# Performance work log

Hardware: AMD Instinct MI355X
Metric: run time of the kernel (lower is better)

The kernel has to match this reference:

```python
import jax, jax.numpy as jnp
import numpy as np

B, C, H, W = 4, 512, 64, 64
C8 = C // 8


def setup_inputs() -> dict:
    key = jax.random.key(0)
    ks = jax.random.split(key, 8)
    s = 0.02
    return {
        "x": jax.random.normal(ks[0], (B, C, H, W), dtype=jnp.float32),
        "wq": jax.random.normal(ks[1], (C8, C), dtype=jnp.float32) * s,
        "bq": jax.random.normal(ks[2], (C8,), dtype=jnp.float32) * s,
        "wk": jax.random.normal(ks[3], (C8, C), dtype=jnp.float32) * s,
        "bk": jax.random.normal(ks[4], (C8,), dtype=jnp.float32) * s,
        "wv": jax.random.normal(ks[5], (C, C), dtype=jnp.float32) * s,
        "bv": jax.random.normal(ks[6], (C,), dtype=jnp.float32) * s,
        "gamma": jax.random.normal(ks[7], (1,), dtype=jnp.float32),
    }


def reference(x, wq, bq, wk, bk, wv, bv, gamma):
    b, c, h, w = x.shape
    # 1x1 convs == per-pixel linear projections
    q = jnp.einsum('bchw,oc->bohw', x, wq) + bq[None, :, None, None]  # [B,C8,H,W]
    k = jnp.einsum('bchw,oc->bohw', x, wk) + bk[None, :, None, None]  # [B,C8,H,W]
    v = jnp.einsum('bchw,oc->bohw', x, wv) + bv[None, :, None, None]  # [B,C,H,W]
    qf = q.reshape(b, c // 8, h * w)  # [B,C8,HW]
    kf = k.reshape(b, c // 8, h * w)  # [B,C8,HW]
    # energy[b,i,j] = q_i . k_j, viewed as [B,H,W,H,W]; softmax over last dim
    energy = jnp.einsum('bci,bcj->bij', qf, kf).reshape(b, h, w, h, w)
    attn = jax.nn.softmax(energy, axis=-1)  # [B,H,W,H2,W2]
    # torch: out = bmm(value, permute(0,1,3,2,4).view(B,HW,HW))
    # rows index (h,h2) into value's spatial grid; cols index output (w,w2)
    out = jnp.einsum('bchk,bhwkv->bcwv', v, attn)  # [B,C,H,W]
    return gamma * out + x
```

## Files before the change

kernel.cpp:

```cpp
#include <hip/hip_runtime.h>
#include <hip/hip_bf16.h>


typedef __bf16 bf16_t;
typedef __bf16 bf16x8 __attribute__((ext_vector_type(8)));
typedef __bf16 bf16x4 __attribute__((ext_vector_type(4)));
typedef float f32x4 __attribute__((ext_vector_type(4)));

#define HW_ 4096
#define CIN 512
#define CQ 64
#define MTOT 640

__device__ __forceinline__ void gload16(const void* g, void* l) {
  __builtin_amdgcn_global_load_lds((const __attribute__((address_space(1))) void*)g,
                                   (__attribute__((address_space(3))) void*)l, 16, 0, 0);
}

__global__ __launch_bounds__(256) void k_wcat(const float* __restrict__ wq,
                                              const float* __restrict__ wk,
                                              const float* __restrict__ wv,
                                              bf16_t* __restrict__ Wcat) {
  int idx = (blockIdx.x * 256 + threadIdx.x) * 4;
  int row = idx >> 9, c = idx & 511;
  const float* src;
  if (row < 64)       src = wq + row * 512 + c;
  else if (row < 128) src = wk + (row - 64) * 512 + c;
  else                src = wv + (row - 128) * 512 + c;
  float4 v = *(const float4*)src;
  bf16x4 o = { (bf16_t)v.x, (bf16_t)v.y, (bf16_t)v.z, (bf16_t)v.w };
  *(bf16x4*)&Wcat[idx] = o;
}

__global__ __launch_bounds__(256) void k_prep(const float* __restrict__ x, bf16_t* __restrict__ xT) {
  __shared__ float tile[64][65];
  const int b = blockIdx.z;
  const int p0 = blockIdx.x * 64, c0 = blockIdx.y * 64;
  const float* xb = x + (size_t)b * CIN * HW_;
  bf16_t* xTb = xT + (size_t)b * HW_ * CIN;
  const int tid = threadIdx.x;
  const int r = tid >> 4, q = tid & 15;
#pragma unroll
  for (int i = 0; i < 4; ++i) {
    int lr = r + 16 * i;
    float4 v = *(const float4*)&xb[(size_t)(c0 + lr) * HW_ + p0 + q * 4];
    tile[lr][q * 4 + 0] = v.x; tile[lr][q * 4 + 1] = v.y;
    tile[lr][q * 4 + 2] = v.z; tile[lr][q * 4 + 3] = v.w;
  }
  __syncthreads();
#pragma unroll
  for (int i = 0; i < 4; ++i) {
    int pr = r + 16 * i;
    bf16x4 o;
    o[0] = (bf16_t)tile[q * 4 + 0][pr];
    o[1] = (bf16_t)tile[q * 4 + 1][pr];
    o[2] = (bf16_t)tile[q * 4 + 2][pr];
    o[3] = (bf16_t)tile[q * 4 + 3][pr];
    *(bf16x4*)&xTb[(size_t)(p0 + pr) * CIN + c0 + q * 4] = o;
  }
}

__global__ __launch_bounds__(256) void k_proj(const bf16_t* __restrict__ Wcat,
                                              const bf16_t* __restrict__ xT,
                                              const float* __restrict__ bq,
                                              const float* __restrict__ bk,
                                              const float* __restrict__ bv,
                                              bf16_t* __restrict__ qfT,
                                              bf16_t* __restrict__ kfT,
                                              bf16_t* __restrict__ Vp) {
  __shared__ bf16_t As[128][64];
  __shared__ bf16_t Bs[128][64];
  const int b = blockIdx.z;
  const int m0 = blockIdx.x * 128, n0 = blockIdx.y * 128;
  const char* Wb = (const char*)Wcat;
  const char* Xb = (const char*)(xT + (size_t)b * HW_ * CIN);
  const int tid = threadIdx.x, wv_ = tid >> 6, lane = tid & 63;
  const int wm = wv_ >> 1, wn = wv_ & 1;
  f32x4 acc[4][4]{};
  for (int ks = 0; ks < 512; ks += 64) {
    if (ks) __syncthreads();
#pragma unroll
    for (int i = 0; i < 4; ++i) {
      int ch = wv_ * 4 + i;
      int rr = ch * 8 + (lane >> 3);
      gload16(Wb + (size_t)(m0 + rr) * 1024 + ks * 2 + (lane & 7) * 16, (char*)As + ch * 1024);
      gload16(Xb + (size_t)(n0 + rr) * 1024 + ks * 2 + (lane & 7) * 16, (char*)Bs + ch * 1024);
    }
    __syncthreads();
#pragma unroll
    for (int k2 = 0; k2 < 2; ++k2) {
      bf16x8 a[4], bb[4];
#pragma unroll
      for (int f = 0; f < 4; ++f)
        a[f] = *(const bf16x8*)&As[wm * 64 + f * 16 + (lane & 15)][k2 * 32 + (lane >> 4) * 8];
#pragma unroll
      for (int f = 0; f < 4; ++f)
        bb[f] = *(const bf16x8*)&Bs[wn * 64 + f * 16 + (lane & 15)][k2 * 32 + (lane >> 4) * 8];
#pragma unroll
      for (int fm = 0; fm < 4; ++fm)
#pragma unroll
        for (int fn = 0; fn < 4; ++fn)
          acc[fm][fn] = __builtin_amdgcn_mfma_f32_16x16x32_bf16(a[fm], bb[fn], acc[fm][fn], 0, 0, 0);
    }
  }
  bf16_t* qb = qfT + (size_t)b * HW_ * CQ;
  bf16_t* kb = kfT + (size_t)b * HW_ * CQ;
  bf16_t* Vb = Vp + (size_t)b * CIN * HW_;
#pragma unroll
  for (int fm = 0; fm < 4; ++fm) {
#pragma unroll
    for (int j = 0; j < 4; ++j) {
      int m = m0 + wm * 64 + fm * 16 + (lane >> 4) * 4 + j;
      float bias = (m < 64) ? bq[m] : (m < 128) ? bk[m - 64] : bv[m - 128];
#pragma unroll
      for (int fn = 0; fn < 4; ++fn) {
        int n = n0 + wn * 64 + fn * 16 + (lane & 15);
        float val = acc[fm][fn][j] + bias;
        if (m < 64)       qb[(size_t)n * CQ + m] = (bf16_t)val;
        else if (m < 128) kb[(size_t)n * CQ + (m - 64)] = (bf16_t)val;
        else              Vb[(size_t)(m - 128) * HW_ + n] = (bf16_t)val;
      }
    }
  }
}

__global__ __launch_bounds__(256) void k_energy(const bf16_t* __restrict__ qfT,
                                                const bf16_t* __restrict__ kfT,
                                                bf16_t* __restrict__ P4, int zbase) {
  __shared__ bf16_t As[128][64];
  __shared__ bf16_t Bs[64][64];
  const int b = zbase + blockIdx.z;
  const int m0 = blockIdx.x * 128, n0 = blockIdx.y * 64;
  const char* qb = (const char*)(qfT + (size_t)b * HW_ * CQ);
  const char* kb = (const char*)(kfT + (size_t)b * HW_ * CQ);
  bf16_t* Pb = P4 + (size_t)blockIdx.z * (size_t)HW_ * HW_;
  const int tid = threadIdx.x, wv_ = tid >> 6, lane = tid & 63;
  f32x4 acc[2][4]{};
#pragma unroll
  for (int i = 0; i < 4; ++i) {
    int ch = wv_ * 4 + i;
    gload16(qb + (size_t)m0 * 128 + ch * 1024 + lane * 16, (char*)As + ch * 1024);
  }
#pragma unroll
  for (int i = 0; i < 2; ++i) {
    int ch = wv_ * 2 + i;
    gload16(kb + (size_t)n0 * 128 + ch * 1024 + lane * 16, (char*)Bs + ch * 1024);
  }
  __syncthreads();
#pragma unroll
  for (int k2 = 0; k2 < 2; ++k2) {
    bf16x8 a[2], bb[4];
#pragma unroll
    for (int f = 0; f < 2; ++f)
      a[f] = *(const bf16x8*)&As[wv_ * 32 + f * 16 + (lane & 15)][k2 * 32 + (lane >> 4) * 8];
#pragma unroll
    for (int f = 0; f < 4; ++f)
      bb[f] = *(const bf16x8*)&Bs[f * 16 + (lane & 15)][k2 * 32 + (lane >> 4) * 8];
#pragma unroll
    for (int fm = 0; fm < 2; ++fm)
#pragma unroll
      for (int fn = 0; fn < 4; ++fn)
        acc[fm][fn] = __builtin_amdgcn_mfma_f32_16x16x32_bf16(a[fm], bb[fn], acc[fm][fn], 0, 0, 0);
  }
#pragma unroll
  for (int fm = 0; fm < 2; ++fm) {
#pragma unroll
    for (int j = 0; j < 4; ++j) {
      float mx = fmaxf(fmaxf(acc[fm][0][j], acc[fm][1][j]), fmaxf(acc[fm][2][j], acc[fm][3][j]));
#pragma unroll
      for (int d = 1; d < 16; d <<= 1) mx = fmaxf(mx, __shfl_xor(mx, d, 64));
      float p0 = __expf(acc[fm][0][j] - mx);
      float p1 = __expf(acc[fm][1][j] - mx);
      float p2 = __expf(acc[fm][2][j] - mx);
      float p3 = __expf(acc[fm][3][j] - mx);
      float s = p0 + p1 + p2 + p3;
#pragma unroll
      for (int d = 1; d < 16; d <<= 1) s += __shfl_xor(s, d, 64);
      float inv = __builtin_amdgcn_rcpf(s);
      size_t hw = (size_t)(m0 + wv_ * 32 + fm * 16 + (lane >> 4) * 4 + j);
      size_t base = hw * HW_ + n0 + (lane & 15);
      Pb[base + 0]  = (bf16_t)(p0 * inv);
      Pb[base + 16] = (bf16_t)(p1 * inv);
      Pb[base + 32] = (bf16_t)(p2 * inv);
      Pb[base + 48] = (bf16_t)(p3 * inv);
    }
  }
}

__global__ __launch_bounds__(256) void k_out(const bf16_t* __restrict__ Vp,
                                             const bf16_t* __restrict__ P4,
                                             const float* __restrict__ x,
                                             const float* __restrict__ gamma,
                                             float* __restrict__ outp, int zbase) {
  __shared__ char As[16384];
  __shared__ char Bs[16384];
  const int b = zbase + blockIdx.z;
  const int c0 = blockIdx.x * 128, w0 = blockIdx.y * 2;
  const char* Vb = (const char*)(Vp + (size_t)b * CIN * HW_);
  const char* Pb = (const char*)(P4 + (size_t)blockIdx.z * (size_t)HW_ * HW_);
  const int tid = threadIdx.x, wv_ = tid >> 6, lane = tid & 63;
  const int wm = wv_ >> 1, wn = wv_ & 1;
  const int g = lane >> 4, cc = lane & 15;

  const char* aS[4]; const char* bS[4]; char* aD[4]; char* bD[4];
#pragma unroll
  for (int r = 0; r < 4; ++r) {
    int L = (r * 4 + wv_) * 64 + lane;
    int arow = L >> 3, aslot = (L & 7) ^ (arow & 7);
    aS[r] = Vb + (size_t)(c0 + arow) * 8192 + aslot * 16;
    int ws = L >> 9, e = L & 511;
    int kk = e >> 3, sl = (e & 7) ^ ((kk >> 3) & 3) << 1;
    bS[r] = Pb + (size_t)(w0 + ws) * 8192 + kk * 128 + sl * 16;
    aD[r] = As + (r * 4 + wv_) * 1024;
    bD[r] = Bs + (r * 4 + wv_) * 1024;
  }
  int aoff[2][4], boff[2][4];
#pragma unroll
  for (int k2 = 0; k2 < 2; ++k2) {
#pragma unroll
    for (int fm = 0; fm < 4; ++fm)
      aoff[k2][fm] = (wm * 64 + fm * 16 + cc) * 128 + (((k2 * 4 + g) ^ (cc & 7)) * 16);
#pragma unroll
    for (int fn = 0; fn < 4; ++fn)
      boff[k2][fn] = wn * 8192 + (k2 * 32 + g * 8) * 128 + (((fn * 16 + cc) ^ (g << 4)) * 2);
  }

  f32x4 acc[4][4]{};
  for (int h = 0; h < 64; ++h) {
#pragma unroll
    for (int r = 0; r < 4; ++r) gload16(aS[r], aD[r]);
#pragma unroll
    for (int r = 0; r < 4; ++r) gload16(bS[r], bD[r]);
#pragma unroll
    for (int r = 0; r < 4; ++r) { aS[r] += 128; bS[r] += 524288; }
    __syncthreads();
#pragma unroll
    for (int k2 = 0; k2 < 2; ++k2) {
      bf16x8 a[4], bb[4];
#pragma unroll
      for (int fm = 0; fm < 4; ++fm)
        a[fm] = *(const bf16x8*)(As + aoff[k2][fm]);
#pragma unroll
      for (int fn = 0; fn < 4; ++fn) {
#pragma unroll
        for (int j = 0; j < 8; ++j)
          bb[fn][j] = *(const bf16_t*)(Bs + boff[k2][fn] + j * 128);
      }
#pragma unroll
      for (int fm = 0; fm < 4; ++fm)
#pragma unroll
        for (int fn = 0; fn < 4; ++fn)
          acc[fm][fn] = __builtin_amdgcn_mfma_f32_16x16x32_bf16(a[fm], bb[fn], acc[fm][fn], 0, 0, 0);
    }
    __syncthreads();
  }
  const float gmm = gamma[0];
  const float* xb = x + (size_t)b * CIN * HW_;
  float* ob = outp + (size_t)b * CIN * HW_;
  const int w = w0 + wn;
#pragma unroll
  for (int fm = 0; fm < 4; ++fm) {
#pragma unroll
    for (int jj = 0; jj < 4; ++jj) {
      int c = c0 + wm * 64 + fm * 16 + g * 4 + jj;
#pragma unroll
      for (int fn = 0; fn < 4; ++fn) {
        int n = w * 64 + fn * 16 + cc;
        size_t idx = (size_t)c * HW_ + n;
        ob[idx] = gmm * acc[fm][fn][jj] + xb[idx];
      }
    }
  }
}

extern "C" void kernel_launch(void* const* d_in, const int* in_sizes, int n_in,
                              void* d_out, int out_size, void* d_ws, size_t ws_size,
                              hipStream_t stream) {
  const float* x  = (const float*)d_in[0];
  const float* wq = (const float*)d_in[1];
  const float* bq = (const float*)d_in[2];
  const float* wk = (const float*)d_in[3];
  const float* bk = (const float*)d_in[4];
  const float* wv = (const float*)d_in[5];
  const float* bv = (const float*)d_in[6];
  const float* gamma = (const float*)d_in[7];
  float* outp = (float*)d_out;
  char* ws = (char*)d_ws;
  size_t off = 0;
  bf16_t* xT   = (bf16_t*)(ws + off); off += (size_t)4 * HW_ * CIN * 2;
  bf16_t* Wcat = (bf16_t*)(ws + off); off += (size_t)MTOT * CIN * 2;
  bf16_t* qfT  = (bf16_t*)(ws + off); off += (size_t)4 * HW_ * CQ * 2;
  bf16_t* kfT  = (bf16_t*)(ws + off); off += (size_t)4 * HW_ * CQ * 2;
  bf16_t* Vp   = (bf16_t*)(ws + off); off += (size_t)4 * CIN * HW_ * 2;
  bf16_t* P4   = (bf16_t*)(ws + off);
  const size_t pbytes = (size_t)HW_ * HW_ * 2;
  const bool full = (ws_size >= off + 4 * pbytes);

  k_wcat<<<dim3(320), dim3(256), 0, stream>>>(wq, wk, wv, Wcat);
  k_prep<<<dim3(64, 8, 4), dim3(256), 0, stream>>>(x, xT);
  k_proj<<<dim3(5, 32, 4), dim3(256), 0, stream>>>(Wcat, xT, bq, bk, bv, qfT, kfT, Vp);
  if (full) {
    k_energy<<<dim3(32, 64, 4), dim3(256), 0, stream>>>(qfT, kfT, P4, 0);
    k_out<<<dim3(4, 32, 4), dim3(256), 0, stream>>>(Vp, P4, x, gamma, outp, 0);
  } else {
    for (int b = 0; b < 4; ++b) {
      k_energy<<<dim3(32, 64, 1), dim3(256), 0, stream>>>(qfT, kfT, P4, b);
      k_out<<<dim3(4, 32, 1), dim3(256), 0, stream>>>(Vp, P4, x, gamma, outp, b);
    }
  }
}
```

Measured before the change: 184.2 us.

## Reorder P and V layouts, swizzle LDS, double-buffer the attention-output GEMM

Splits the projection into separate Q/K and V kernels. The V kernel writes V with pixels permuted so the k_out reduction reads contiguous rows. k_energy now stores the softmax probabilities transposed in a [w][ky][v][h] layout, so k_out can load both operands as 16-byte vectors instead of gathering scalar bf16 values. All GEMM LDS tiles use an XOR swizzle to reduce bank conflicts, and k_out gains a double-buffered prefetch pipeline with explicit waitcnt and barriers. The cost is more complex indexing, strided 8-byte stores in the energy kernel, and a larger LDS footprint in k_out.

```diff
diff --git a/kernel.cpp b/kernel.cpp
--- a/kernel.cpp
+++ b/kernel.cpp
@@ -10,7 +10,6 @@
 #define HW_ 4096
 #define CIN 512
 #define CQ 64
-#define MTOT 640
 
 __device__ __forceinline__ void gload16(const void* g, void* l) {
   __builtin_amdgcn_global_load_lds((const __attribute__((address_space(1))) void*)g,
@@ -60,22 +59,21 @@
   }
 }
 
-__global__ __launch_bounds__(256) void k_proj(const bf16_t* __restrict__ Wcat,
-                                              const bf16_t* __restrict__ xT,
-                                              const float* __restrict__ bq,
-                                              const float* __restrict__ bk,
-                                              const float* __restrict__ bv,
-                                              bf16_t* __restrict__ qfT,
-                                              bf16_t* __restrict__ kfT,
-                                              bf16_t* __restrict__ Vp) {
+__global__ __launch_bounds__(256) void k_projqk(const bf16_t* __restrict__ Wcat,
+                                                const bf16_t* __restrict__ xT,
+                                                const float* __restrict__ bq,
+                                                const float* __restrict__ bk,
+                                                bf16_t* __restrict__ qfT,
+                                                bf16_t* __restrict__ kfT) {
   __shared__ bf16_t As[128][64];
   __shared__ bf16_t Bs[128][64];
   const int b = blockIdx.z;
-  const int m0 = blockIdx.x * 128, n0 = blockIdx.y * 128;
+  const int n0 = blockIdx.x * 128;
   const char* Wb = (const char*)Wcat;
   const char* Xb = (const char*)(xT + (size_t)b * HW_ * CIN);
   const int tid = threadIdx.x, wv_ = tid >> 6, lane = tid & 63;
   const int wm = wv_ >> 1, wn = wv_ & 1;
+  const int g = lane >> 4, cc = lane & 15;
   f32x4 acc[4][4]{};
   for (int ks = 0; ks < 512; ks += 64) {
     if (ks) __syncthreads();
@@ -83,8 +81,9 @@
     for (int i = 0; i < 4; ++i) {
       int ch = wv_ * 4 + i;
       int rr = ch * 8 + (lane >> 3);
-      gload16(Wb + (size_t)(m0 + rr) * 1024 + ks * 2 + (lane & 7) * 16, (char*)As + ch * 1024);
-      gload16(Xb + (size_t)(n0 + rr) * 1024 + ks * 2 + (lane & 7) * 16, (char*)Bs + ch * 1024);
+      int sl = (lane & 7) ^ (rr & 7);
+      gload16(Wb + (size_t)rr * 1024 + ks * 2 + sl * 16, (char*)As + ch * 1024);
+      gload16(Xb + (size_t)(n0 + rr) * 1024 + ks * 2 + sl * 16, (char*)Bs + ch * 1024);
     }
     __syncthreads();
 #pragma unroll
@@ -92,10 +91,10 @@
       bf16x8 a[4], bb[4];
 #pragma unroll
       for (int f = 0; f < 4; ++f)
-        a[f] = *(const bf16x8*)&As[wm * 64 + f * 16 + (lane & 15)][k2 * 32 + (lane >> 4) * 8];
+        a[f] = *(const bf16x8*)((char*)As + (wm * 64 + f * 16 + cc) * 128 + (((k2 * 4 + g) ^ (cc & 7)) * 16));
 #pragma unroll
       for (int f = 0; f < 4; ++f)
-        bb[f] = *(const bf16x8*)&Bs[wn * 64 + f * 16 + (lane & 15)][k2 * 32 + (lane >> 4) * 8];
+        bb[f] = *(const bf16x8*)((char*)Bs + (wn * 64 + f * 16 + cc) * 128 + (((k2 * 4 + g) ^ (cc & 7)) * 16));
 #pragma unroll
       for (int fm = 0; fm < 4; ++fm)
 #pragma unroll
@@ -105,20 +104,76 @@
   }
   bf16_t* qb = qfT + (size_t)b * HW_ * CQ;
   bf16_t* kb = kfT + (size_t)b * HW_ * CQ;
-  bf16_t* Vb = Vp + (size_t)b * CIN * HW_;
 #pragma unroll
   for (int fm = 0; fm < 4; ++fm) {
 #pragma unroll
     for (int j = 0; j < 4; ++j) {
-      int m = m0 + wm * 64 + fm * 16 + (lane >> 4) * 4 + j;
-      float bias = (m < 64) ? bq[m] : (m < 128) ? bk[m - 64] : bv[m - 128];
+      int m = wm * 64 + fm * 16 + g * 4 + j;
+      float bias = (m < 64) ? bq[m] : bk[m - 64];
 #pragma unroll
       for (int fn = 0; fn < 4; ++fn) {
-        int n = n0 + wn * 64 + fn * 16 + (lane & 15);
+        int n = n0 + wn * 64 + fn * 16 + cc;
         float val = acc[fm][fn][j] + bias;
-        if (m < 64)       qb[(size_t)n * CQ + m] = (bf16_t)val;
-        else if (m < 128) kb[(size_t)n * CQ + (m - 64)] = (bf16_t)val;
-        else              Vb[(size_t)(m - 128) * HW_ + n] = (bf16_t)val;
+        if (m < 64) qb[(size_t)n * CQ + m] = (bf16_t)val;
+        else        kb[(size_t)n * CQ + (m - 64)] = (bf16_t)val;
+      }
+    }
+  }
+}
+
+__global__ __launch_bounds__(256) void k_projv(const bf16_t* __restrict__ Wcat,
+                                               const bf16_t* __restrict__ xT,
+                                               const float* __restrict__ bv,
+                                               bf16_t* __restrict__ Vp2) {
+  __shared__ bf16_t As[128][64];
+  __shared__ bf16_t Bs[128][64];
+  const int b = blockIdx.z;
+  const int n0 = blockIdx.x * 128, m0 = blockIdx.y * 128;
+  const char* Wb = (const char*)Wcat;
+  const char* Xb = (const char*)(xT + (size_t)b * HW_ * CIN);
+  const int tid = threadIdx.x, wv_ = tid >> 6, lane = tid & 63;
+  const int wm = wv_ >> 1, wn = wv_ & 1;
+  const int g = lane >> 4, cc = lane & 15;
+  f32x4 acc[4][4]{};
+  for (int ks = 0; ks < 512; ks += 64) {
+    if (ks) __syncthreads();
+#pragma unroll
+    for (int i = 0; i < 4; ++i) {
+      int ch = wv_ * 4 + i;
+      int rr = ch * 8 + (lane >> 3);
+      int sl = (lane & 7) ^ (rr & 7);
+      int pix = (rr & 63) * 64 + (blockIdx.x * 2) + (rr >> 6);
+      gload16(Wb + (size_t)(128 + m0 + rr) * 1024 + ks * 2 + sl * 16, (char*)As + ch * 1024);
+      gload16(Xb + (size_t)pix * 1024 + ks * 2 + sl * 16, (char*)Bs + ch * 1024);
+    }
+    __syncthreads();
+#pragma unroll
+    for (int k2 = 0; k2 < 2; ++k2) {
+      bf16x8 a[4], bb[4];
+#pragma unroll
+      for (int f = 0; f < 4; ++f)
+        a[f] = *(const bf16x8*)((char*)As + (wm * 64 + f * 16 + cc) * 128 + (((k2 * 4 + g) ^ (cc & 7)) * 16));
+#pragma unroll
+      for (int f = 0; f < 4; ++f)
+        bb[f] = *(const bf16x8*)((char*)Bs + (wn * 64 + f * 16 + cc) * 128 + (((k2 * 4 + g) ^ (cc & 7)) * 16));
+#pragma unroll
+      for (int fm = 0; fm < 4; ++fm)
+#pragma unroll
+        for (int fn = 0; fn < 4; ++fn)
+          acc[fm][fn] = __builtin_amdgcn_mfma_f32_16x16x32_bf16(a[fm], bb[fn], acc[fm][fn], 0, 0, 0);
+    }
+  }
+  bf16_t* Vb = Vp2 + (size_t)b * CIN * HW_;
+#pragma unroll
+  for (int fm = 0; fm < 4; ++fm) {
+#pragma unroll
+    for (int j = 0; j < 4; ++j) {
+      int m = m0 + wm * 64 + fm * 16 + g * 4 + j;
+      float bias = bv[m];
+#pragma unroll
+      for (int fn = 0; fn < 4; ++fn) {
+        int n = n0 + wn * 64 + fn * 16 + cc;
+        Vb[(size_t)m * HW_ + n] = (bf16_t)(acc[fm][fn][j] + bias);
       }
     }
   }
@@ -126,25 +181,31 @@
 
 __global__ __launch_bounds__(256) void k_energy(const bf16_t* __restrict__ qfT,
                                                 const bf16_t* __restrict__ kfT,
-                                                bf16_t* __restrict__ P4, int zbase) {
+                                                bf16_t* __restrict__ Pt, int zbase) {
   __shared__ bf16_t As[128][64];
   __shared__ bf16_t Bs[64][64];
   const int b = zbase + blockIdx.z;
-  const int m0 = blockIdx.x * 128, n0 = blockIdx.y * 64;
+  const int w0 = blockIdx.x * 2, ky = blockIdx.y;
   const char* qb = (const char*)(qfT + (size_t)b * HW_ * CQ);
   const char* kb = (const char*)(kfT + (size_t)b * HW_ * CQ);
-  bf16_t* Pb = P4 + (size_t)blockIdx.z * (size_t)HW_ * HW_;
+  bf16_t* Ptb = Pt + (size_t)blockIdx.z * 16777216;
   const int tid = threadIdx.x, wv_ = tid >> 6, lane = tid & 63;
+  const int g = lane >> 4, cc = lane & 15;
   f32x4 acc[2][4]{};
 #pragma unroll
   for (int i = 0; i < 4; ++i) {
     int ch = wv_ * 4 + i;
-    gload16(qb + (size_t)m0 * 128 + ch * 1024 + lane * 16, (char*)As + ch * 1024);
+    int rr = ch * 8 + (lane >> 3);
+    int sl = (lane & 7) ^ (rr & 7);
+    int pix = (rr & 63) * 64 + w0 + (rr >> 6);
+    gload16(qb + (size_t)pix * 128 + sl * 16, (char*)As + ch * 1024);
   }
 #pragma unroll
   for (int i = 0; i < 2; ++i) {
     int ch = wv_ * 2 + i;
-    gload16(kb + (size_t)n0 * 128 + ch * 1024 + lane * 16, (char*)Bs + ch * 1024);
+    int rr = ch * 8 + (lane >> 3);
+    int sl = (lane & 7) ^ (rr & 7);
+    gload16(kb + (size_t)(ky * 64 + rr) * 128 + sl * 16, (char*)Bs + ch * 1024);
   }
   __syncthreads();
 #pragma unroll
@@ -152,67 +213,65 @@
     bf16x8 a[2], bb[4];
 #pragma unroll
     for (int f = 0; f < 2; ++f)
-      a[f] = *(const bf16x8*)&As[wv_ * 32 + f * 16 + (lane & 15)][k2 * 32 + (lane >> 4) * 8];
+      a[f] = *(const bf16x8*)((char*)As + (wv_ * 32 + f * 16 + cc) * 128 + (((k2 * 4 + g) ^ (cc & 7)) * 16));
 #pragma unroll
     for (int f = 0; f < 4; ++f)
-      bb[f] = *(const bf16x8*)&Bs[f * 16 + (lane & 15)][k2 * 32 + (lane >> 4) * 8];
+      bb[f] = *(const bf16x8*)((char*)Bs + (f * 16 + cc) * 128 + (((k2 * 4 + g) ^ (cc & 7)) * 16));
 #pragma unroll
     for (int fm = 0; fm < 2; ++fm)
 #pragma unroll
       for (int fn = 0; fn < 4; ++fn)
         acc[fm][fn] = __builtin_amdgcn_mfma_f32_16x16x32_bf16(a[fm], bb[fn], acc[fm][fn], 0, 0, 0);
   }
+  const int w = w0 + (wv_ >> 1);
 #pragma unroll
   for (int fm = 0; fm < 2; ++fm) {
+    float e[4][4], invj[4];
 #pragma unroll
     for (int j = 0; j < 4; ++j) {
       float mx = fmaxf(fmaxf(acc[fm][0][j], acc[fm][1][j]), fmaxf(acc[fm][2][j], acc[fm][3][j]));
 #pragma unroll
       for (int d = 1; d < 16; d <<= 1) mx = fmaxf(mx, __shfl_xor(mx, d, 64));
-      float p0 = __expf(acc[fm][0][j] - mx);
-      float p1 = __expf(acc[fm][1][j] - mx);
-      float p2 = __expf(acc[fm][2][j] - mx);
-      float p3 = __expf(acc[fm][3][j] - mx);
-      float s = p0 + p1 + p2 + p3;
+      float s = 0.f;
+#pragma unroll
+      for (int fn = 0; fn < 4; ++fn) { e[fn][j] = __expf(acc[fm][fn][j] - mx); s += e[fn][j]; }
 #pragma unroll
       for (int d = 1; d < 16; d <<= 1) s += __shfl_xor(s, d, 64);
-      float inv = __builtin_amdgcn_rcpf(s);
-      size_t hw = (size_t)(m0 + wv_ * 32 + fm * 16 + (lane >> 4) * 4 + j);
-      size_t base = hw * HW_ + n0 + (lane & 15);
-      Pb[base + 0]  = (bf16_t)(p0 * inv);
-      Pb[base + 16] = (bf16_t)(p1 * inv);
-      Pb[base + 32] = (bf16_t)(p2 * inv);
-      Pb[base + 48] = (bf16_t)(p3 * inv);
-    }
-  }
-}
-
-__global__ __launch_bounds__(256) void k_out(const bf16_t* __restrict__ Vp,
-                                             const bf16_t* __restrict__ P4,
+      invj[j] = __builtin_amdgcn_rcpf(s);
+    }
+    int h0 = (wv_ & 1) * 32 + fm * 16 + g * 4;
+#pragma unroll
+    for (int fn = 0; fn < 4; ++fn) {
+      int v = fn * 16 + cc;
+      bf16x4 pk = { (bf16_t)(e[fn][0] * invj[0]), (bf16_t)(e[fn][1] * invj[1]),
+                    (bf16_t)(e[fn][2] * invj[2]), (bf16_t)(e[fn][3] * invj[3]) };
+      *(bf16x4*)&Ptb[(((size_t)w * 64 + ky) * 64 + v) * 64 + h0] = pk;
+    }
+  }
+}
+
+__global__ __launch_bounds__(256) void k_out(const bf16_t* __restrict__ Vp2,
+                                             const bf16_t* __restrict__ Pt,
                                              const float* __restrict__ x,
                                              const float* __restrict__ gamma,
                                              float* __restrict__ outp, int zbase) {
-  __shared__ char As[16384];
-  __shared__ char Bs[16384];
+  __shared__ char Ls[65536];
   const int b = zbase + blockIdx.z;
   const int c0 = blockIdx.x * 128, w0 = blockIdx.y * 2;
-  const char* Vb = (const char*)(Vp + (size_t)b * CIN * HW_);
-  const char* Pb = (const char*)(P4 + (size_t)blockIdx.z * (size_t)HW_ * HW_);
+  const char* Vb = (const char*)(Vp2 + (size_t)b * CIN * HW_);
+  const char* Pb = (const char*)(Pt + (size_t)blockIdx.z * 16777216);
   const int tid = threadIdx.x, wv_ = tid >> 6, lane = tid & 63;
   const int wm = wv_ >> 1, wn = wv_ & 1;
   const int g = lane >> 4, cc = lane & 15;
 
-  const char* aS[4]; const char* bS[4]; char* aD[4]; char* bD[4];
+  const char* aSb[4]; const char* bSb[4];
 #pragma unroll
   for (int r = 0; r < 4; ++r) {
     int L = (r * 4 + wv_) * 64 + lane;
-    int arow = L >> 3, aslot = (L & 7) ^ (arow & 7);
-    aS[r] = Vb + (size_t)(c0 + arow) * 8192 + aslot * 16;
-    int ws = L >> 9, e = L & 511;
-    int kk = e >> 3, sl = (e & 7) ^ ((kk >> 3) & 3) << 1;
-    bS[r] = Pb + (size_t)(w0 + ws) * 8192 + kk * 128 + sl * 16;
-    aD[r] = As + (r * 4 + wv_) * 1024;
-    bD[r] = Bs + (r * 4 + wv_) * 1024;
+    int arow = L >> 3, asl = (L & 7) ^ (arow & 7);
+    aSb[r] = Vb + (size_t)(c0 + arow) * 8192 + asl * 16;
+    int ws = L >> 9, e = L & 511, v = e >> 3, bsl = (e & 7) ^ (v & 7);
+    bSb[r] = Pb + (size_t)(w0 + ws) * 524288 + v * 128 + bsl * 16;
   }
   int aoff[2][4], boff[2][4];
 #pragma unroll
@@ -222,37 +281,45 @@
       aoff[k2][fm] = (wm * 64 + fm * 16 + cc) * 128 + (((k2 * 4 + g) ^ (cc & 7)) * 16);
 #pragma unroll
     for (int fn = 0; fn < 4; ++fn)
-      boff[k2][fn] = wn * 8192 + (k2 * 32 + g * 8) * 128 + (((fn * 16 + cc) ^ (g << 4)) * 2);
+      boff[k2][fn] = 16384 + wn * 8192 + (fn * 16 + cc) * 128 + (((k2 * 4 + g) ^ (cc & 7)) * 16);
   }
 
   f32x4 acc[4][4]{};
-  for (int h = 0; h < 64; ++h) {
-#pragma unroll
-    for (int r = 0; r < 4; ++r) gload16(aS[r], aD[r]);
-#pragma unroll
-    for (int r = 0; r < 4; ++r) gload16(bS[r], bD[r]);
-#pragma unroll
-    for (int r = 0; r < 4; ++r) { aS[r] += 128; bS[r] += 524288; }
-    __syncthreads();
+  {
+    char* base = Ls;
+#pragma unroll
+    for (int r = 0; r < 4; ++r) gload16(aSb[r], base + (r * 4 + wv_) * 1024);
+#pragma unroll
+    for (int r = 0; r < 4; ++r) gload16(bSb[r], base + 16384 + (r * 4 + wv_) * 1024);
+  }
+  for (int s = 0; s < 64; ++s) {
+    if (s < 63) {
+      char* base = Ls + ((s + 1) & 1) * 32768;
+#pragma unroll
+      for (int r = 0; r < 4; ++r) gload16(aSb[r] + (size_t)(s + 1) * 128, base + (r * 4 + wv_) * 1024);
+#pragma unroll
+      for (int r = 0; r < 4; ++r) gload16(bSb[r] + (size_t)(s + 1) * 8192, base + 16384 + (r * 4 + wv_) * 1024);
+      asm volatile("s_waitcnt vmcnt(8)" ::: "memory");
+    } else {
+      asm volatile("s_waitcnt vmcnt(0)" ::: "memory");
+    }
+    __builtin_amdgcn_s_barrier();
+    const char* base = Ls + (s & 1) * 32768;
 #pragma unroll
     for (int k2 = 0; k2 < 2; ++k2) {
       bf16x8 a[4], bb[4];
 #pragma unroll
-      for (int fm = 0; fm < 4; ++fm)
-        a[fm] = *(const bf16x8*)(As + aoff[k2][fm]);
-#pragma unroll
-      for (int fn = 0; fn < 4; ++fn) {
-#pragma unroll
-        for (int j = 0; j < 8; ++j)
-          bb[fn][j] = *(const bf16_t*)(Bs + boff[k2][fn] + j * 128);
-      }
+      for (int fm = 0; fm < 4; ++fm) a[fm] = *(const bf16x8*)(base + aoff[k2][fm]);
+#pragma unroll
+      for (int fn = 0; fn < 4; ++fn) bb[fn] = *(const bf16x8*)(base + boff[k2][fn]);
 #pragma unroll
       for (int fm = 0; fm < 4; ++fm)
 #pragma unroll
         for (int fn = 0; fn < 4; ++fn)
           acc[fm][fn] = __builtin_amdgcn_mfma_f32_16x16x32_bf16(a[fm], bb[fn], acc[fm][fn], 0, 0, 0);
     }
-    __syncthreads();
+    asm volatile("s_waitcnt lgkmcnt(0)" ::: "memory");
+    __builtin_amdgcn_s_barrier();
   }
   const float gmm = gamma[0];
   const float* xb = x + (size_t)b * CIN * HW_;
@@ -288,24 +355,25 @@
   char* ws = (char*)d_ws;
   size_t off = 0;
   bf16_t* xT   = (bf16_t*)(ws + off); off += (size_t)4 * HW_ * CIN * 2;
-  bf16_t* Wcat = (bf16_t*)(ws + off); off += (size_t)MTOT * CIN * 2;
+  bf16_t* Wcat = (bf16_t*)(ws + off); off += (size_t)640 * CIN * 2;
   bf16_t* qfT  = (bf16_t*)(ws + off); off += (size_t)4 * HW_ * CQ * 2;
   bf16_t* kfT  = (bf16_t*)(ws + off); off += (size_t)4 * HW_ * CQ * 2;
-  bf16_t* Vp   = (bf16_t*)(ws + off); off += (size_t)4 * CIN * HW_ * 2;
-  bf16_t* P4   = (bf16_t*)(ws + off);
+  bf16_t* Vp2  = (bf16_t*)(ws + off); off += (size_t)4 * CIN * HW_ * 2;
+  bf16_t* Pt   = (bf16_t*)(ws + off);
   const size_t pbytes = (size_t)HW_ * HW_ * 2;
   const bool full = (ws_size >= off + 4 * pbytes);
 
   k_wcat<<<dim3(320), dim3(256), 0, stream>>>(wq, wk, wv, Wcat);
   k_prep<<<dim3(64, 8, 4), dim3(256), 0, stream>>>(x, xT);
-  k_proj<<<dim3(5, 32, 4), dim3(256), 0, stream>>>(Wcat, xT, bq, bk, bv, qfT, kfT, Vp);
+  k_projqk<<<dim3(32, 1, 4), dim3(256), 0, stream>>>(Wcat, xT, bq, bk, qfT, kfT);
+  k_projv<<<dim3(32, 4, 4), dim3(256), 0, stream>>>(Wcat, xT, bv, Vp2);
   if (full) {
-    k_energy<<<dim3(32, 64, 4), dim3(256), 0, stream>>>(qfT, kfT, P4, 0);
-    k_out<<<dim3(4, 32, 4), dim3(256), 0, stream>>>(Vp, P4, x, gamma, outp, 0);
+    k_energy<<<dim3(32, 64, 4), dim3(256), 0, stream>>>(qfT, kfT, Pt, 0);
+    k_out<<<dim3(4, 32, 4), dim3(256), 0, stream>>>(Vp2, Pt, x, gamma, outp, 0);
   } else {
     for (int b = 0; b < 4; ++b) {
-      k_energy<<<dim3(32, 64, 1), dim3(256), 0, stream>>>(qfT, kfT, P4, b);
-      k_out<<<dim3(4, 32, 1), dim3(256), 0, stream>>>(Vp, P4, x, gamma, outp, b);
-    }
-  }
-}
+      k_energy<<<dim3(32, 64, 1), dim3(256), 0, stream>>>(qfT, kfT, Pt, b);
+      k_out<<<dim3(4, 32, 1), dim3(256), 0, stream>>>(Vp2, Pt, x, gamma, outp, b);
+    }
+  }
+}
```

Result: slower. 190.7 us (+3.5%).
